# Kernel optimization log

Measured on AMD Instinct MI355X. Metric: run time of the kernel, lower is better.

## Reference

```python
import jax, jax.numpy as jnp
import numpy as np

N_NODES = 100000
N_EDGES = 1600000
IN_FEATS = 128
HID = 32
N_REL = 5
N_BASES = 2
N_PAIRS = 4096


def setup_inputs() -> dict:
    key = jax.random.key(0)
    ks = jax.random.split(key, 24)
    d = {}
    d['x'] = jax.random.normal(ks[0], (N_NODES, IN_FEATS), dtype=jnp.float32)
    d['edge_mask'] = jnp.ones((N_EDGES,), dtype=jnp.float32)
    d['etype'] = jax.random.randint(ks[1], (N_EDGES,), 0, N_REL, dtype=jnp.int32)
    d['src'] = jax.random.randint(ks[2], (N_EDGES,), 0, N_NODES, dtype=jnp.int32)
    d['dst'] = jax.random.randint(ks[3], (N_EDGES,), 0, N_NODES, dtype=jnp.int32)
    d['users_idx'] = jax.random.randint(ks[4], (N_PAIRS,), 0, N_NODES, dtype=jnp.int32)
    d['items_idx'] = jax.random.randint(ks[5], (N_PAIRS,), 0, N_NODES, dtype=jnp.int32)
    # RelGraphConv params (basis decomposition): layer1 in->32, layers 2,3 32->32
    def s(k, din):
        return 1.0 / np.sqrt(din)
    d['V1'] = jax.random.normal(ks[6], (N_BASES, IN_FEATS, HID), dtype=jnp.float32) * s(0, IN_FEATS)
    d['comp1'] = jax.random.normal(ks[7], (N_REL, N_BASES), dtype=jnp.float32)
    d['loop1'] = jax.random.normal(ks[8], (IN_FEATS, HID), dtype=jnp.float32) * s(0, IN_FEATS)
    d['b1'] = jnp.zeros((HID,), dtype=jnp.float32)
    d['V2'] = jax.random.normal(ks[9], (N_BASES, HID, HID), dtype=jnp.float32) * s(0, HID)
    d['comp2'] = jax.random.normal(ks[10], (N_REL, N_BASES), dtype=jnp.float32)
    d['loop2'] = jax.random.normal(ks[11], (HID, HID), dtype=jnp.float32) * s(0, HID)
    d['b2'] = jnp.zeros((HID,), dtype=jnp.float32)
    d['V3'] = jax.random.normal(ks[12], (N_BASES, HID, HID), dtype=jnp.float32) * s(0, HID)
    d['comp3'] = jax.random.normal(ks[13], (N_REL, N_BASES), dtype=jnp.float32)
    d['loop3'] = jax.random.normal(ks[14], (HID, HID), dtype=jnp.float32) * s(0, HID)
    d['b3'] = jnp.zeros((HID,), dtype=jnp.float32)
    # MLP head: lin1 (2*sum(latent_dim[1:]) = 192 -> 128), lin2 (128 -> 1)
    d['w1'] = jax.random.normal(ks[15], (2 * 3 * HID, 128), dtype=jnp.float32) * (1.0 / np.sqrt(2 * 3 * HID))
    d['bw1'] = jnp.zeros((128,), dtype=jnp.float32)
    d['w2'] = jax.random.normal(ks[16], (128, 1), dtype=jnp.float32) * (1.0 / np.sqrt(128))
    d['bw2'] = jnp.zeros((1,), dtype=jnp.float32)
    return d


def _rgcn_layer(x, V, comp, loopw, bias, etype, src, dst, norm):
    # basis-decomposed relational conv: W_r = sum_b comp[r,b] * V[b]
    xb = jnp.einsum('nd,bdo->nbo', x, V)                       # [N,B,O]
    msg = jnp.einsum('eb,ebo->eo', comp[etype], xb[src])       # [E,O]
    msg = msg * norm[:, None]                                  # edge_mask norm
    agg = jax.ops.segment_sum(msg, dst, num_segments=x.shape[0])
    return jnp.tanh(agg + x @ loopw + bias)


def reference(x, edge_mask, etype, src, dst, users_idx, items_idx,
              V1, comp1, loop1, b1, V2, comp2, loop2, b2, V3, comp3, loop3, b3,
              w1, bw1, w2, bw2):
    h1 = _rgcn_layer(x, V1, comp1, loop1, b1, etype, src, dst, edge_mask)
    h2 = _rgcn_layer(h1, V2, comp2, loop2, b2, etype, src, dst, edge_mask)
    h3 = _rgcn_layer(h2, V3, comp3, loop3, b3, etype, src, dst, edge_mask)
    concat_states = jnp.concatenate([h1, h2, h3], axis=1)      # [N, 96]
    feats = jnp.concatenate([concat_states[users_idx], concat_states[items_idx]], axis=1)  # [P,192]
    hidden = jax.nn.relu(feats @ w1 + bw1)
    out = hidden @ w2 + bw2
    return out[:, 0]  # multiply_by = 1
```

## Files before the change

### kernel.cpp

```cpp
#include <hip/hip_runtime.h>
#include <stdint.h>

#define N_NODES  100000
#define N_EDGES  1600000
#define IN_FEATS 128
#define HID      32
#define N_REL    5
#define N_BASES  2
#define N_PAIRS  4096

#define NB        196
#define BCAP      16384
#define EPB       2048
#define SC_BLOCKS 782
#define TL1_BLOCKS 1250
#define NGROUPS   6250

typedef __attribute__((ext_vector_type(8))) short short8;
typedef __attribute__((ext_vector_type(4))) float f32x4;

__device__ inline unsigned int pack_bf16(float a, float b) {
    unsigned int ua = __float_as_uint(a), ub = __float_as_uint(b);
    ua = (ua + 0x7fffu + ((ua >> 16) & 1u)) >> 16;
    ub = (ub + 0x7fffu + ((ub >> 16) & 1u)) >> 16;
    return ua | (ub << 16);
}

__device__ inline unsigned short bf16_1(float a) {
    unsigned int u = __float_as_uint(a);
    u = (u + 0x7fffu + ((u >> 16) & 1u)) >> 16;
    return (unsigned short)u;
}

__device__ inline void split_bf16_2(float a, float b, unsigned int& hi, unsigned int& lo) {
    unsigned int ha = bf16_1(a), hb = bf16_1(b);
    hi = ha | (hb << 16);
    float fa = __uint_as_float(ha << 16), fb = __uint_as_float(hb << 16);
    lo = pack_bf16(a - fa, b - fb);
}


__global__ __launch_bounds__(256) void k_wprep(
    const float* __restrict__ V1, const float* __restrict__ comp1, const float* __restrict__ loop1,
    const float* __restrict__ V2, const float* __restrict__ loop2,
    const float* __restrict__ V3, const float* __restrict__ loop3,
    unsigned short* __restrict__ Wbf1, unsigned short* __restrict__ Wcat2,
    unsigned short* __restrict__ Wcat3, int* __restrict__ gcur) {
    int b = blockIdx.x;
    int t = threadIdx.x;
    if (b == 0 && t < NB) gcur[t] = 0;
    if (b < 96) {
        int idx = b * 256 + t;
        if (idx >= 192 * IN_FEATS) return;
        int j = idx / IN_FEATS, k = idx % IN_FEATS;
        float v;
        if (j < 160) {
            int r = j >> 5, o = j & 31;
            v = comp1[r * 2 + 0] * V1[(size_t)(0 * IN_FEATS + k) * 32 + o]
              + comp1[r * 2 + 1] * V1[(size_t)(1 * IN_FEATS + k) * 32 + o];
        } else {
            v = loop1[k * 32 + (j - 160)];
        }
        Wbf1[idx] = bf16_1(v);
        return;
    }
    const float *V, *loopw;
    unsigned short* Wc;
    int idx;
    if (b < 116) { V = V2; loopw = loop2; Wc = Wcat2; idx = (b - 96) * 256 + t; }
    else         { V = V3; loopw = loop3; Wc = Wcat3; idx = (b - 116) * 256 + t; }
    if (idx >= 32 * 160) return;
    int col = idx / 160, k = idx % 160;
    int seg = k >> 5, inner = k & 31;
    float v;
    if (seg < 2)      v = V[inner * 32 + col];
    else if (seg < 4) v = V[(32 + inner) * 32 + col];
    else              v = loopw[inner * 32 + col];
    Wc[idx] = bf16_1(v);
}


__global__ __launch_bounds__(256) void k_fused1(
    const int* __restrict__ src, const int* __restrict__ dst,
    const int* __restrict__ etype, const float* __restrict__ mask,
    int* __restrict__ gcur, int2* __restrict__ ebuf,
    const float* __restrict__ xin,
    const unsigned short* __restrict__ Wbf, const float* __restrict__ bias,
    unsigned short* __restrict__ xs16, float* __restrict__ aggout) {
    int b = blockIdx.x;
    int t = threadIdx.x;
    if (b < SC_BLOCKS) {
        __shared__ int lh[NB];
        __shared__ int lex[NB];
        __shared__ int gbase[NB];
        __shared__ int scanbuf[256];
        __shared__ int2  srec[EPB];
        __shared__ short sb[EPB];
        int e0 = b * EPB;
        if (t < NB) lh[t] = 0;
        __syncthreads();
        int2 rec[8];
        int  bk[8];
#pragma unroll
        for (int i = 0; i < 8; i++) {
            int e = e0 + t + i * 256;
            if (e < N_EDGES) {
                int d = dst[e];
                bk[i] = d >> 9;
                rec[i].x = ((d & 511) << 23) | (src[e] << 4) | etype[e];
                rec[i].y = __float_as_int(mask[e]);
                atomicAdd(&lh[bk[i]], 1);
            } else bk[i] = -1;
        }
        __syncthreads();
        int cnt = (t < NB) ? lh[t] : 0;
        scanbuf[t] = cnt;
        __syncthreads();
        for (int off = 1; off < 256; off <<= 1) {
            int v = (t >= off) ? scanbuf[t - off] : 0;
            __syncthreads();
            scanbuf[t] += v;
            __syncthreads();
        }
        if (t < NB) {
            lex[t] = scanbuf[t] - cnt;
            gbase[t] = t * BCAP + (cnt ? atomicAdd(&gcur[t], cnt) : 0);
            lh[t] = 0;
        }
        __syncthreads();
#pragma unroll
        for (int i = 0; i < 8; i++) {
            if (bk[i] >= 0) {
                int p = lex[bk[i]] + atomicAdd(&lh[bk[i]], 1);
                srec[p] = rec[i];
                sb[p] = (short)bk[i];
            }
        }
        __syncthreads();
        int total = scanbuf[NB - 1];
        for (int idx = t; idx < total; idx += 256) {
            int bb = sb[idx];
            ebuf[gbase[bb] + (idx - lex[bb])] = srec[idx];
        }
        return;
    }
    __shared__ unsigned short As[16 * 136];
    int bb = b - SC_BLOCKS;
    int wv = t >> 6, lane = t & 63;
    int q = lane >> 4, n16 = lane & 15;
    short8 bfr[3][4];
#pragma unroll
    for (int i = 0; i < 3; i++) {
        int tt = wv * 3 + i;
#pragma unroll
        for (int ks = 0; ks < 4; ks++)
            bfr[i][ks] = *(const short8*)(Wbf + (tt * 16 + n16) * 128 + ks * 32 + q * 8);
    }
    float bv0 = bias[n16], bv1 = bias[16 + n16];
    int node_l = t >> 4;
    int seg    = t & 15;
    int g0 = bb * 5;
    float4 p0, p1;
    {
        const float* xr = xin + ((size_t)(g0 * 16 + node_l)) * 128 + seg * 8;
        p0 = *(const float4*)xr;
        p1 = *(const float4*)(xr + 4);
    }
    for (int gi = 0; gi < 5; gi++) {
        int g = g0 + gi;
        int n0 = g * 16;
        __syncthreads();
        {
            unsigned int u0 = pack_bf16(p0.x, p0.y);
            unsigned int u1 = pack_bf16(p0.z, p0.w);
            unsigned int u2 = pack_bf16(p1.x, p1.y);
            unsigned int u3 = pack_bf16(p1.z, p1.w);
            uint4 v; v.x = u0; v.y = u1; v.z = u2; v.w = u3;
            *(uint4*)(As + node_l * 136 + seg * 8) = v;
        }
        __syncthreads();
        if (gi + 1 < 5) {
            const float* xr = xin + ((size_t)((g + 1) * 16 + node_l)) * 128 + seg * 8;
            p0 = *(const float4*)xr;
            p1 = *(const float4*)(xr + 4);
        }
        short8 afr[4];
#pragma unroll
        for (int ks = 0; ks < 4; ks++)
            afr[ks] = *(const short8*)(As + n16 * 136 + ks * 32 + q * 8);
        f32x4 d[3];
        f32x4 z = {0.f, 0.f, 0.f, 0.f};
#pragma unroll
        for (int i = 0; i < 3; i++) d[i] = z;
#pragma unroll
        for (int i = 0; i < 3; i++)
#pragma unroll
            for (int ks = 0; ks < 4; ks++)
                d[i] = __builtin_amdgcn_mfma_f32_16x16x32_bf16(afr[ks], bfr[i][ks], d[i], 0, 0, 0);
#pragma unroll
        for (int i = 0; i < 3; i++) {
            int tt = wv * 3 + i;
            if (tt < 10) {
#pragma unroll
                for (int r = 0; r < 4; r++) {
                    int node = n0 + q * 4 + r;
                    xs16[(size_t)node * 160 + tt * 16 + n16] = bf16_1(d[i][r]);
                }
            } else {
                float bv = (tt == 10) ? bv0 : bv1;
                int o = (tt - 10) * 16 + n16;
#pragma unroll
                for (int r = 0; r < 4; r++) {
                    int node = n0 + q * 4 + r;
                    aggout[(size_t)node * 32 + o] = d[i][r] + bv;
                }
            }
        }
    }
}


__global__ __launch_bounds__(512) void k_bsort2(
    const int* __restrict__ gcur, const int2* __restrict__ ebuf,
    int2* __restrict__ esort, int* __restrict__ offsets) {
    __shared__ int hist[512];
    __shared__ int incl[512];
    __shared__ int cur[512];
    __shared__ int bs[256];
    __shared__ int sBase, sCnt;
    int blk = blockIdx.x, b = blk >> 1, h = blk & 1, t = threadIdx.x;
    if (t < 256) bs[t] = (t < NB) ? gcur[t] : 0;
    __syncthreads();
    for (int off = 1; off < 256; off <<= 1) {
        int v = 0;
        if (t < 256 && t >= off) v = bs[t - off];
        __syncthreads();
        if (t < 256) bs[t] += v;
        __syncthreads();
    }
    if (t == 0) { sCnt = gcur[b]; sBase = bs[b] - gcur[b]; }
    hist[t] = 0;
    __syncthreads();
    int cnt = sCnt, gbase = sBase;
    const int2* slab = ebuf + (size_t)b * BCAP;
    for (int e = t; e < cnt; e += 512) {
        int dl = ((unsigned)slab[e].x) >> 23;
        atomicAdd(&hist[dl], 1);
    }
    __syncthreads();
    incl[t] = hist[t];
    __syncthreads();
    for (int off = 1; off < 512; off <<= 1) {
        int v = 0;
        if (t >= off) v = incl[t - off];
        __syncthreads();
        incl[t] += v;
        __syncthreads();
    }
    int ex = incl[t] - hist[t];
    cur[t] = ex;
    if ((t >> 8) == h) {
        int n = (b << 9) + t;
        if (n <= N_NODES) offsets[n] = gbase + ex;
    }
    if (b == NB - 1 && h == 1 && t == 0) offsets[N_NODES] = N_EDGES;
    __syncthreads();
    for (int e = t; e < cnt; e += 512) {
        int2 pk = slab[e];
        int dl = ((unsigned)pk.x) >> 23;
        if ((dl >> 8) == h) {
            int pos = gbase + atomicAdd(&cur[dl], 1);
            int2 rec;
            rec.x = pk.x & 0x7fffff;
            rec.y = pk.y;
            esort[pos] = rec;
        }
    }
}


__global__ __launch_bounds__(256) void k_agg1(
    const int* __restrict__ offsets, const int2* __restrict__ esort,
    const unsigned int* __restrict__ xrel16, const float* __restrict__ agg,
    float* __restrict__ concat, unsigned int* __restrict__ hrel_out) {
    int v = blockIdx.x * 32 + (threadIdx.x >> 3);
    int o = threadIdx.x & 7;
    int s0 = offsets[v], s1 = offsets[v + 1];
    float4 a0 = *(const float4*)(agg + (size_t)v * 32 + o * 4);
    float acc0 = a0.x, acc1 = a0.y, acc2 = a0.z, acc3 = a0.w;
    int last = s1 - 1;
    for (int e = s0; e < s1; e += 16) {
        int addr[16];
        float m[16];
#pragma unroll
        for (int i = 0; i < 16; i++) {
            int ei = e + i;
            int ec = (ei <= last) ? ei : last;
            int2 pk = esort[ec];
            int low = pk.x;
            addr[i] = (low >> 4) * 80 + (low & 15) * 16;
            m[i] = (ei <= last) ? __int_as_float(pk.y) : 0.f;
        }
        uint2 xw[16];
#pragma unroll
        for (int i = 0; i < 16; i++)
            xw[i] = *(const uint2*)(xrel16 + (unsigned)addr[i] + o * 2);
#pragma unroll
        for (int i = 0; i < 16; i++) {
            float f0 = __uint_as_float(xw[i].x << 16);
            float f1 = __uint_as_float(xw[i].x & 0xffff0000u);
            float f2 = __uint_as_float(xw[i].y << 16);
            float f3 = __uint_as_float(xw[i].y & 0xffff0000u);
            acc0 = fmaf(m[i], f0, acc0);
            acc1 = fmaf(m[i], f1, acc1);
            acc2 = fmaf(m[i], f2, acc2);
            acc3 = fmaf(m[i], f3, acc3);
        }
    }
    float4 r;
    r.x = tanhf(acc0); r.y = tanhf(acc1); r.z = tanhf(acc2); r.w = tanhf(acc3);
    *(float4*)(concat + (size_t)v * 96 + o * 4) = r;
    hrel_out[v * 16 + o * 2]     = pack_bf16(r.x, r.y);
    hrel_out[v * 16 + o * 2 + 1] = pack_bf16(r.z, r.w);
}


__global__ __launch_bounds__(256) void k_agg23(
    const int* __restrict__ offsets, const int2* __restrict__ esort,
    const unsigned int* __restrict__ hrel_in, const float* __restrict__ comp,
    const unsigned short* __restrict__ Wcat, const float* __restrict__ bias,
    float* __restrict__ concat, int hoff, unsigned int* __restrict__ hrel_out) {
    __shared__ unsigned int hbf[32][84];
    __shared__ float2 cLds[5];
    int t = threadIdx.x;
    if (t < 5) cLds[t] = ((const float2*)comp)[t];
    int nl = t >> 3;
    int v = blockIdx.x * 32 + nl;
    int o = t & 7;
    int s0 = offsets[v], s1 = offsets[v + 1];
    __syncthreads();
    float y00 = 0.f, y01 = 0.f, y02 = 0.f, y03 = 0.f;
    float y10 = 0.f, y11 = 0.f, y12 = 0.f, y13 = 0.f;
    int last = s1 - 1;
    for (int e = s0; e < s1; e += 16) {
        int addr[16];
        float c0[16], c1[16];
#pragma unroll
        for (int i = 0; i < 16; i++) {
            int ei = e + i;
            int ec = (ei <= last) ? ei : last;
            int2 pk = esort[ec];
            int low = pk.x;
            addr[i] = low & 0x7ffff0;
            float2 cc = cLds[low & 15];
            float m = (ei <= last) ? __int_as_float(pk.y) : 0.f;
            c0[i] = m * cc.x;
            c1[i] = m * cc.y;
        }
        uint2 xw[16];
#pragma unroll
        for (int i = 0; i < 16; i++)
            xw[i] = *(const uint2*)(hrel_in + (unsigned)addr[i] + o * 2);
#pragma unroll
        for (int i = 0; i < 16; i++) {
            float f0 = __uint_as_float(xw[i].x << 16);
            float f1 = __uint_as_float(xw[i].x & 0xffff0000u);
            float f2 = __uint_as_float(xw[i].y << 16);
            float f3 = __uint_as_float(xw[i].y & 0xffff0000u);
            y00 = fmaf(c0[i], f0, y00); y10 = fmaf(c1[i], f0, y10);
            y01 = fmaf(c0[i], f1, y01); y11 = fmaf(c1[i], f1, y11);
            y02 = fmaf(c0[i], f2, y02); y12 = fmaf(c1[i], f2, y12);
            y03 = fmaf(c0[i], f3, y03); y13 = fmaf(c1[i], f3, y13);
        }
    }
    unsigned int hi, lo;
    split_bf16_2(y00, y01, hi, lo);
    hbf[nl][o * 2]          = hi;  hbf[nl][16 + o * 2]     = lo;
    split_bf16_2(y02, y03, hi, lo);
    hbf[nl][o * 2 + 1]      = hi;  hbf[nl][16 + o * 2 + 1] = lo;
    split_bf16_2(y10, y11, hi, lo);
    hbf[nl][32 + o * 2]     = hi;  hbf[nl][48 + o * 2]     = lo;
    split_bf16_2(y12, y13, hi, lo);
    hbf[nl][32 + o * 2 + 1] = hi;  hbf[nl][48 + o * 2 + 1] = lo;
    *(uint2*)&hbf[nl][64 + o * 2] = *(const uint2*)(hrel_in + v * 16 + o * 2);
    __syncthreads();
    int wv = t >> 6, lane = t & 63;
    int q = lane >> 4, n16 = lane & 15;
    int gg = wv & 1;
    int tt = wv >> 1;
    f32x4 d = {0.f, 0.f, 0.f, 0.f};
#pragma unroll
    for (int ks = 0; ks < 5; ks++) {
        short8 afr = *(const short8*)&hbf[gg * 16 + n16][ks * 16 + q * 4];
        short8 bfr = *(const short8*)(Wcat + (tt * 16 + n16) * 160 + ks * 32 + q * 8);
        d = __builtin_amdgcn_mfma_f32_16x16x32_bf16(afr, bfr, d, 0, 0, 0);
    }
    float bv = bias[tt * 16 + n16];
    int n0 = blockIdx.x * 32 + gg * 16;
#pragma unroll
    for (int r = 0; r < 4; r++) {
        int node = n0 + q * 4 + r;
        float h = tanhf(d[r] + bv);
        concat[(size_t)node * 96 + hoff + tt * 16 + n16] = h;
        if (hrel_out)
            ((unsigned short*)hrel_out)[node * 32 + tt * 16 + n16] = bf16_1(h);
    }
}


__global__ void k_mlp(const float* __restrict__ concat, const int* __restrict__ uidx,
                      const int* __restrict__ iidx,
                      const float* __restrict__ w1, const float* __restrict__ bw1,
                      const float* __restrict__ w2, const float* __restrict__ bw2,
                      float* __restrict__ out) {
    __shared__ float feats[192];
    __shared__ float red[2];
    int p = blockIdx.x;
    int t = threadIdx.x;
    int u = uidx[p], it = iidx[p];
    for (int k = t; k < 192; k += 128)
        feats[k] = (k < 96) ? concat[(size_t)u * 96 + k] : concat[(size_t)it * 96 + (k - 96)];
    __syncthreads();
    float acc = bw1[t];
    for (int k = 0; k < 192; k++) acc += feats[k] * w1[k * 128 + t];
    float h = fmaxf(acc, 0.f);
    float part = h * w2[t];
    for (int off = 32; off > 0; off >>= 1) part += __shfl_down(part, off, 64);
    if ((t & 63) == 0) red[t >> 6] = part;
    __syncthreads();
    if (t == 0) out[p] = red[0] + red[1] + bw2[0];
}


extern "C" void kernel_launch(void* const* d_in, const int* in_sizes, int n_in,
                              void* d_out, int out_size, void* d_ws, size_t ws_size,
                              hipStream_t stream) {
    const float* x         = (const float*)d_in[0];
    const float* edge_mask = (const float*)d_in[1];
    const int*   etype     = (const int*)d_in[2];
    const int*   src       = (const int*)d_in[3];
    const int*   dst       = (const int*)d_in[4];
    const int*   users_idx = (const int*)d_in[5];
    const int*   items_idx = (const int*)d_in[6];
    const float* V1        = (const float*)d_in[7];
    const float* comp1     = (const float*)d_in[8];
    const float* loop1     = (const float*)d_in[9];
    const float* b1        = (const float*)d_in[10];
    const float* V2        = (const float*)d_in[11];
    const float* comp2     = (const float*)d_in[12];
    const float* loop2     = (const float*)d_in[13];
    const float* b2        = (const float*)d_in[14];
    const float* V3        = (const float*)d_in[15];
    const float* comp3     = (const float*)d_in[16];
    const float* loop3     = (const float*)d_in[17];
    const float* b3        = (const float*)d_in[18];
    const float* w1        = (const float*)d_in[19];
    const float* bw1       = (const float*)d_in[20];
    const float* w2        = (const float*)d_in[21];
    const float* bw2       = (const float*)d_in[22];
    float* out = (float*)d_out;

    uintptr_t w = (uintptr_t)d_ws;
    auto al = [&](size_t bytes) { uintptr_t p = (w + 255) & ~(uintptr_t)255; w = p + bytes; return p; };
    int*   gcur    = (int*)al(sizeof(int) * NB);
    int*   offsets = (int*)al(sizeof(int) * (N_NODES + 1));
    int2*  ebuf    = (int2*)al(sizeof(int2) * (size_t)NB * BCAP);
    unsigned int* xs16  = (unsigned int*)al(sizeof(unsigned int) * (size_t)N_NODES * 80);
    unsigned int* hrel1 = (unsigned int*)al(sizeof(unsigned int) * (size_t)N_NODES * 16);
    unsigned int* hrel2 = (unsigned int*)al(sizeof(unsigned int) * (size_t)N_NODES * 16);
    int2*  esort   = (int2*)al(sizeof(int2) * N_EDGES);
    unsigned short* Wbf1  = (unsigned short*)al(sizeof(unsigned short) * 192 * IN_FEATS);
    unsigned short* Wcat2 = (unsigned short*)al(sizeof(unsigned short) * 32 * 160);
    unsigned short* Wcat3 = (unsigned short*)al(sizeof(unsigned short) * 32 * 160);
    float* aggA    = (float*)al(sizeof(float) * (size_t)N_NODES * 32);
    float* concat  = (float*)al(sizeof(float) * (size_t)N_NODES * 96);

    k_wprep<<<136, 256, 0, stream>>>(V1, comp1, loop1, V2, loop2, V3, loop3,
                                     Wbf1, Wcat2, Wcat3, gcur);
    k_fused1<<<SC_BLOCKS + TL1_BLOCKS, 256, 0, stream>>>(
        src, dst, etype, edge_mask, gcur, ebuf,
        x, Wbf1, b1, (unsigned short*)xs16, aggA);
    k_bsort2<<<2 * NB, 512, 0, stream>>>(gcur, ebuf, esort, offsets);

    const int agrid = N_NODES / 32;

    k_agg1<<<agrid, 256, 0, stream>>>(offsets, esort, xs16, aggA, concat, hrel1);
    k_agg23<<<agrid, 256, 0, stream>>>(offsets, esort, hrel1, comp2, Wcat2, b2,
                                       concat, 32, hrel2);
    k_agg23<<<agrid, 256, 0, stream>>>(offsets, esort, hrel2, comp3, Wcat3, b3,
                                       concat, 64, (unsigned int*)nullptr);

    k_mlp<<<N_PAIRS, 128, 0, stream>>>(concat, users_idx, items_idx, w1, bw1, w2, bw2, out);
}
```

Before: 318.5 us.

## Widen per-thread gathers in aggregation kernels and scatter edges directly

The aggregation kernels now map 4 threads per node instead of 8, with 64 nodes per block. Each thread does 16-byte bf16 gathers covering 8 features, and the edge loop unrolls by 8. The MFMA stage in k_agg23 has each wave compute both 16-column tiles for its 16 nodes. The edge bucketing in k_fused1 drops the local prefix scan and shared staging, writing records straight to global buckets via LDS atomics. The aim is fewer edge-record loads per feature and wider memory transactions, at the cost of uncoalesced bucket writes, less per-node parallelism and bounds checks for the partial last block.

```diff
diff --git a/kernel.cpp b/kernel.cpp
--- a/kernel.cpp
+++ b/kernel.cpp
@@ -14,7 +14,7 @@
 #define EPB       2048
 #define SC_BLOCKS 782
 #define TL1_BLOCKS 1250
-#define NGROUPS   6250
+#define AGG_GRID  1563
 
 typedef __attribute__((ext_vector_type(8))) short short8;
 typedef __attribute__((ext_vector_type(4))) float f32x4;
@@ -91,11 +91,7 @@
     int t = threadIdx.x;
     if (b < SC_BLOCKS) {
         __shared__ int lh[NB];
-        __shared__ int lex[NB];
         __shared__ int gbase[NB];
-        __shared__ int scanbuf[256];
-        __shared__ int2  srec[EPB];
-        __shared__ short sb[EPB];
         int e0 = b * EPB;
         if (t < NB) lh[t] = 0;
         __syncthreads();
@@ -113,17 +109,8 @@
             } else bk[i] = -1;
         }
         __syncthreads();
-        int cnt = (t < NB) ? lh[t] : 0;
-        scanbuf[t] = cnt;
-        __syncthreads();
-        for (int off = 1; off < 256; off <<= 1) {
-            int v = (t >= off) ? scanbuf[t - off] : 0;
-            __syncthreads();
-            scanbuf[t] += v;
-            __syncthreads();
-        }
         if (t < NB) {
-            lex[t] = scanbuf[t] - cnt;
+            int cnt = lh[t];
             gbase[t] = t * BCAP + (cnt ? atomicAdd(&gcur[t], cnt) : 0);
             lh[t] = 0;
         }
@@ -131,16 +118,9 @@
 #pragma unroll
         for (int i = 0; i < 8; i++) {
             if (bk[i] >= 0) {
-                int p = lex[bk[i]] + atomicAdd(&lh[bk[i]], 1);
-                srec[p] = rec[i];
-                sb[p] = (short)bk[i];
+                int p = atomicAdd(&lh[bk[i]], 1);
+                ebuf[gbase[bk[i]] + p] = rec[i];
             }
-        }
-        __syncthreads();
-        int total = scanbuf[NB - 1];
-        for (int idx = t; idx < total; idx += 256) {
-            int bb = sb[idx];
-            ebuf[gbase[bb] + (idx - lex[bb])] = srec[idx];
         }
         return;
     }
@@ -283,17 +263,29 @@
     const int* __restrict__ offsets, const int2* __restrict__ esort,
     const unsigned int* __restrict__ xrel16, const float* __restrict__ agg,
     float* __restrict__ concat, unsigned int* __restrict__ hrel_out) {
-    int v = blockIdx.x * 32 + (threadIdx.x >> 3);
-    int o = threadIdx.x & 7;
-    int s0 = offsets[v], s1 = offsets[v + 1];
-    float4 a0 = *(const float4*)(agg + (size_t)v * 32 + o * 4);
-    float acc0 = a0.x, acc1 = a0.y, acc2 = a0.z, acc3 = a0.w;
+    int t = threadIdx.x;
+    int nl = t >> 2;
+    int v = blockIdx.x * 64 + nl;
+    int o = t & 3;
+    bool valid = v < N_NODES;
+    int s0 = 0, s1 = 0;
+    if (valid) { s0 = offsets[v]; s1 = offsets[v + 1]; }
+    float acc[8];
+    if (valid) {
+        float4 a0 = *(const float4*)(agg + (size_t)v * 32 + o * 8);
+        float4 a1 = *(const float4*)(agg + (size_t)v * 32 + o * 8 + 4);
+        acc[0] = a0.x; acc[1] = a0.y; acc[2] = a0.z; acc[3] = a0.w;
+        acc[4] = a1.x; acc[5] = a1.y; acc[6] = a1.z; acc[7] = a1.w;
+    } else {
+#pragma unroll
+        for (int i = 0; i < 8; i++) acc[i] = 0.f;
+    }
     int last = s1 - 1;
-    for (int e = s0; e < s1; e += 16) {
-        int addr[16];
-        float m[16];
-#pragma unroll
-        for (int i = 0; i < 16; i++) {
+    for (int e = s0; e < s1; e += 8) {
+        int addr[8];
+        float m[8];
+#pragma unroll
+        for (int i = 0; i < 8; i++) {
             int ei = e + i;
             int ec = (ei <= last) ? ei : last;
             int2 pk = esort[ec];
@@ -301,27 +293,36 @@
             addr[i] = (low >> 4) * 80 + (low & 15) * 16;
             m[i] = (ei <= last) ? __int_as_float(pk.y) : 0.f;
         }
-        uint2 xw[16];
-#pragma unroll
-        for (int i = 0; i < 16; i++)
-            xw[i] = *(const uint2*)(xrel16 + (unsigned)addr[i] + o * 2);
-#pragma unroll
-        for (int i = 0; i < 16; i++) {
-            float f0 = __uint_as_float(xw[i].x << 16);
-            float f1 = __uint_as_float(xw[i].x & 0xffff0000u);
-            float f2 = __uint_as_float(xw[i].y << 16);
-            float f3 = __uint_as_float(xw[i].y & 0xffff0000u);
-            acc0 = fmaf(m[i], f0, acc0);
-            acc1 = fmaf(m[i], f1, acc1);
-            acc2 = fmaf(m[i], f2, acc2);
-            acc3 = fmaf(m[i], f3, acc3);
-        }
-    }
-    float4 r;
-    r.x = tanhf(acc0); r.y = tanhf(acc1); r.z = tanhf(acc2); r.w = tanhf(acc3);
-    *(float4*)(concat + (size_t)v * 96 + o * 4) = r;
-    hrel_out[v * 16 + o * 2]     = pack_bf16(r.x, r.y);
-    hrel_out[v * 16 + o * 2 + 1] = pack_bf16(r.z, r.w);
+        uint4 xw[8];
+#pragma unroll
+        for (int i = 0; i < 8; i++)
+            xw[i] = *(const uint4*)(xrel16 + (unsigned)addr[i] + o * 4);
+#pragma unroll
+        for (int i = 0; i < 8; i++) {
+            acc[0] = fmaf(m[i], __uint_as_float(xw[i].x << 16), acc[0]);
+            acc[1] = fmaf(m[i], __uint_as_float(xw[i].x & 0xffff0000u), acc[1]);
+            acc[2] = fmaf(m[i], __uint_as_float(xw[i].y << 16), acc[2]);
+            acc[3] = fmaf(m[i], __uint_as_float(xw[i].y & 0xffff0000u), acc[3]);
+            acc[4] = fmaf(m[i], __uint_as_float(xw[i].z << 16), acc[4]);
+            acc[5] = fmaf(m[i], __uint_as_float(xw[i].z & 0xffff0000u), acc[5]);
+            acc[6] = fmaf(m[i], __uint_as_float(xw[i].w << 16), acc[6]);
+            acc[7] = fmaf(m[i], __uint_as_float(xw[i].w & 0xffff0000u), acc[7]);
+        }
+    }
+    if (valid) {
+        float r[8];
+#pragma unroll
+        for (int i = 0; i < 8; i++) r[i] = tanhf(acc[i]);
+        float4 w0, w1;
+        w0.x = r[0]; w0.y = r[1]; w0.z = r[2]; w0.w = r[3];
+        w1.x = r[4]; w1.y = r[5]; w1.z = r[6]; w1.w = r[7];
+        *(float4*)(concat + (size_t)v * 96 + o * 8) = w0;
+        *(float4*)(concat + (size_t)v * 96 + o * 8 + 4) = w1;
+        uint4 hw;
+        hw.x = pack_bf16(r[0], r[1]); hw.y = pack_bf16(r[2], r[3]);
+        hw.z = pack_bf16(r[4], r[5]); hw.w = pack_bf16(r[6], r[7]);
+        *(uint4*)(hrel_out + v * 16 + o * 4) = hw;
+    }
 }
 
 
@@ -330,23 +331,26 @@
     const unsigned int* __restrict__ hrel_in, const float* __restrict__ comp,
     const unsigned short* __restrict__ Wcat, const float* __restrict__ bias,
     float* __restrict__ concat, int hoff, unsigned int* __restrict__ hrel_out) {
-    __shared__ unsigned int hbf[32][84];
+    __shared__ unsigned int hbf[64][84];
     __shared__ float2 cLds[5];
     int t = threadIdx.x;
     if (t < 5) cLds[t] = ((const float2*)comp)[t];
-    int nl = t >> 3;
-    int v = blockIdx.x * 32 + nl;
-    int o = t & 7;
-    int s0 = offsets[v], s1 = offsets[v + 1];
-    __syncthreads();
-    float y00 = 0.f, y01 = 0.f, y02 = 0.f, y03 = 0.f;
-    float y10 = 0.f, y11 = 0.f, y12 = 0.f, y13 = 0.f;
+    int nl = t >> 2;
+    int v = blockIdx.x * 64 + nl;
+    int o = t & 3;
+    bool valid = v < N_NODES;
+    int s0 = 0, s1 = 0;
+    if (valid) { s0 = offsets[v]; s1 = offsets[v + 1]; }
+    __syncthreads();
+    float y0[8], y1[8];
+#pragma unroll
+    for (int i = 0; i < 8; i++) { y0[i] = 0.f; y1[i] = 0.f; }
     int last = s1 - 1;
-    for (int e = s0; e < s1; e += 16) {
-        int addr[16];
-        float c0[16], c1[16];
-#pragma unroll
-        for (int i = 0; i < 16; i++) {
+    for (int e = s0; e < s1; e += 8) {
+        int addr[8];
+        float c0[8], c1[8];
+#pragma unroll
+        for (int i = 0; i < 8; i++) {
             int ei = e + i;
             int ec = (ei <= last) ? ei : last;
             int2 pk = esort[ec];
@@ -357,53 +361,76 @@
             c0[i] = m * cc.x;
             c1[i] = m * cc.y;
         }
-        uint2 xw[16];
-#pragma unroll
-        for (int i = 0; i < 16; i++)
-            xw[i] = *(const uint2*)(hrel_in + (unsigned)addr[i] + o * 2);
-#pragma unroll
-        for (int i = 0; i < 16; i++) {
+        uint4 xw[8];
+#pragma unroll
+        for (int i = 0; i < 8; i++)
+            xw[i] = *(const uint4*)(hrel_in + (unsigned)addr[i] + o * 4);
+#pragma unroll
+        for (int i = 0; i < 8; i++) {
             float f0 = __uint_as_float(xw[i].x << 16);
             float f1 = __uint_as_float(xw[i].x & 0xffff0000u);
             float f2 = __uint_as_float(xw[i].y << 16);
             float f3 = __uint_as_float(xw[i].y & 0xffff0000u);
-            y00 = fmaf(c0[i], f0, y00); y10 = fmaf(c1[i], f0, y10);
-            y01 = fmaf(c0[i], f1, y01); y11 = fmaf(c1[i], f1, y11);
-            y02 = fmaf(c0[i], f2, y02); y12 = fmaf(c1[i], f2, y12);
-            y03 = fmaf(c0[i], f3, y03); y13 = fmaf(c1[i], f3, y13);
-        }
-    }
-    unsigned int hi, lo;
-    split_bf16_2(y00, y01, hi, lo);
-    hbf[nl][o * 2]          = hi;  hbf[nl][16 + o * 2]     = lo;
-    split_bf16_2(y02, y03, hi, lo);
-    hbf[nl][o * 2 + 1]      = hi;  hbf[nl][16 + o * 2 + 1] = lo;
-    split_bf16_2(y10, y11, hi, lo);
-    hbf[nl][32 + o * 2]     = hi;  hbf[nl][48 + o * 2]     = lo;
-    split_bf16_2(y12, y13, hi, lo);
-    hbf[nl][32 + o * 2 + 1] = hi;  hbf[nl][48 + o * 2 + 1] = lo;
-    *(uint2*)&hbf[nl][64 + o * 2] = *(const uint2*)(hrel_in + v * 16 + o * 2);
+            float f4 = __uint_as_float(xw[i].z << 16);
+            float f5 = __uint_as_float(xw[i].z & 0xffff0000u);
+            float f6 = __uint_as_float(xw[i].w << 16);
+            float f7 = __uint_as_float(xw[i].w & 0xffff0000u);
+            y0[0] = fmaf(c0[i], f0, y0[0]); y1[0] = fmaf(c1[i], f0, y1[0]);
+            y0[1] = fmaf(c0[i], f1, y0[1]); y1[1] = fmaf(c1[i], f1, y1[1]);
+            y0[2] = fmaf(c0[i], f2, y0[2]); y1[2] = fmaf(c1[i], f2, y1[2]);
+            y0[3] = fmaf(c0[i], f3, y0[3]); y1[3] = fmaf(c1[i], f3, y1[3]);
+            y0[4] = fmaf(c0[i], f4, y0[4]); y1[4] = fmaf(c1[i], f4, y1[4]);
+            y0[5] = fmaf(c0[i], f5, y0[5]); y1[5] = fmaf(c1[i], f5, y1[5]);
+            y0[6] = fmaf(c0[i], f6, y0[6]); y1[6] = fmaf(c1[i], f6, y1[6]);
+            y0[7] = fmaf(c0[i], f7, y0[7]); y1[7] = fmaf(c1[i], f7, y1[7]);
+        }
+    }
+    {
+        uint4 hi, lo;
+        split_bf16_2(y0[0], y0[1], hi.x, lo.x);
+        split_bf16_2(y0[2], y0[3], hi.y, lo.y);
+        split_bf16_2(y0[4], y0[5], hi.z, lo.z);
+        split_bf16_2(y0[6], y0[7], hi.w, lo.w);
+        *(uint4*)&hbf[nl][o * 4]      = hi;
+        *(uint4*)&hbf[nl][16 + o * 4] = lo;
+        split_bf16_2(y1[0], y1[1], hi.x, lo.x);
+        split_bf16_2(y1[2], y1[3], hi.y, lo.y);
+        split_bf16_2(y1[4], y1[5], hi.z, lo.z);
+        split_bf16_2(y1[6], y1[7], hi.w, lo.w);
+        *(uint4*)&hbf[nl][32 + o * 4] = hi;
+        *(uint4*)&hbf[nl][48 + o * 4] = lo;
+        uint4 hv = {0u, 0u, 0u, 0u};
+        if (valid) hv = *(const uint4*)(hrel_in + v * 16 + o * 4);
+        *(uint4*)&hbf[nl][64 + o * 4] = hv;
+    }
     __syncthreads();
     int wv = t >> 6, lane = t & 63;
     int q = lane >> 4, n16 = lane & 15;
-    int gg = wv & 1;
-    int tt = wv >> 1;
-    f32x4 d = {0.f, 0.f, 0.f, 0.f};
+    f32x4 d0 = {0.f, 0.f, 0.f, 0.f};
+    f32x4 d1 = {0.f, 0.f, 0.f, 0.f};
 #pragma unroll
     for (int ks = 0; ks < 5; ks++) {
-        short8 afr = *(const short8*)&hbf[gg * 16 + n16][ks * 16 + q * 4];
-        short8 bfr = *(const short8*)(Wcat + (tt * 16 + n16) * 160 + ks * 32 + q * 8);
-        d = __builtin_amdgcn_mfma_f32_16x16x32_bf16(afr, bfr, d, 0, 0, 0);
-    }
-    float bv = bias[tt * 16 + n16];
-    int n0 = blockIdx.x * 32 + gg * 16;
+        short8 afr = *(const short8*)&hbf[wv * 16 + n16][ks * 16 + q * 4];
+        short8 b0  = *(const short8*)(Wcat + (n16) * 160 + ks * 32 + q * 8);
+        short8 b1  = *(const short8*)(Wcat + (16 + n16) * 160 + ks * 32 + q * 8);
+        d0 = __builtin_amdgcn_mfma_f32_16x16x32_bf16(afr, b0, d0, 0, 0, 0);
+        d1 = __builtin_amdgcn_mfma_f32_16x16x32_bf16(afr, b1, d1, 0, 0, 0);
+    }
+    float bv0 = bias[n16], bv1 = bias[16 + n16];
+    int n0 = blockIdx.x * 64 + wv * 16;
 #pragma unroll
     for (int r = 0; r < 4; r++) {
         int node = n0 + q * 4 + r;
-        float h = tanhf(d[r] + bv);
-        concat[(size_t)node * 96 + hoff + tt * 16 + n16] = h;
-        if (hrel_out)
-            ((unsigned short*)hrel_out)[node * 32 + tt * 16 + n16] = bf16_1(h);
+        if (node < N_NODES) {
+            float h0 = tanhf(d0[r] + bv0);
+            float h1 = tanhf(d1[r] + bv1);
+            concat[(size_t)node * 96 + hoff + n16]      = h0;
+            concat[(size_t)node * 96 + hoff + 16 + n16] = h1;
+            if (hrel_out) {
+                ((unsigned short*)hrel_out)[node * 32 + n16]      = bf16_1(h0);
+                ((unsigned short*)hrel_out)[node * 32 + 16 + n16] = bf16_1(h1);
+            }
+        }
     }
 }
 
@@ -482,13 +509,11 @@
         x, Wbf1, b1, (unsigned short*)xs16, aggA);
     k_bsort2<<<2 * NB, 512, 0, stream>>>(gcur, ebuf, esort, offsets);
 
-    const int agrid = N_NODES / 32;
-
-    k_agg1<<<agrid, 256, 0, stream>>>(offsets, esort, xs16, aggA, concat, hrel1);
-    k_agg23<<<agrid, 256, 0, stream>>>(offsets, esort, hrel1, comp2, Wcat2, b2,
-                                       concat, 32, hrel2);
-    k_agg23<<<agrid, 256, 0, stream>>>(offsets, esort, hrel2, comp3, Wcat3, b3,
-                                       concat, 64, (unsigned int*)nullptr);
+    k_agg1<<<AGG_GRID, 256, 0, stream>>>(offsets, esort, xs16, aggA, concat, hrel1);
+    k_agg23<<<AGG_GRID, 256, 0, stream>>>(offsets, esort, hrel1, comp2, Wcat2, b2,
+                                          concat, 32, hrel2);
+    k_agg23<<<AGG_GRID, 256, 0, stream>>>(offsets, esort, hrel2, comp3, Wcat3, b3,
+                                          concat, 64, (unsigned int*)nullptr);
 
     k_mlp<<<N_PAIRS, 128, 0, stream>>>(concat, users_idx, items_idx, w1, bw1, w2, bw2, out);
 }
```

New measurement: 330.8 us. 1.04x slower.
